# Performance work log

Measured on AMD Instinct MI355X. Metric: run time of the kernel, lower is better.

## Reference

```python
import jax, jax.numpy as jnp
import numpy as np

N_NODES = 50000
N_EDGES = 800000
NUM_REL = 3
NUM_GRAPHS = 512


def _rgcn(x, src, dst, edge_type, Wrel, Wroot, b):
    # PyG RGCNConv with default aggr='mean':
    # out[i] = x[i] @ Wroot + b + sum_r mean_{j in N_r(i)} x[j] @ Wrel[r]
    out = x @ Wroot + b
    for r in range(NUM_REL):
        mask = (edge_type == r)
        h = x @ Wrel[r]                      # transform nodes first (N x d), cheaper than per-edge
        msg = jnp.where(mask[:, None], h[src], jnp.zeros((), x.dtype))  # [E, hid]
        sums = jax.ops.segment_sum(msg, dst, num_segments=N_NODES)
        cnt = jax.ops.segment_sum(mask.astype(x.dtype), dst, num_segments=N_NODES)
        out = out + sums / jnp.maximum(cnt, 1.0)[:, None]
    return out


def setup_inputs() -> dict:
    key = jax.random.key(0)
    ks = jax.random.split(key, 12)
    d, hid, classes = 96, 96, 16
    x = jax.random.normal(ks[0], (N_NODES, d), dtype=jnp.float32)
    edge_index = jax.random.randint(ks[1], (2, N_EDGES), 0, N_NODES, dtype=jnp.int64)
    edge_type = jax.random.randint(ks[2], (N_EDGES,), 0, NUM_REL, dtype=jnp.int64)
    batch = jnp.sort(jax.random.randint(ks[3], (N_NODES,), 0, NUM_GRAPHS, dtype=jnp.int64))
    s1 = 1.0 / np.sqrt(d)
    s2 = 1.0 / np.sqrt(hid)
    return {
        "x": x,
        "edge_index": edge_index,
        "edge_type": edge_type,
        "batch": batch,
        "Wrel1": jax.random.normal(ks[4], (NUM_REL, d, hid), dtype=jnp.float32) * s1,
        "Wroot1": jax.random.normal(ks[5], (d, hid), dtype=jnp.float32) * s1,
        "b1": jnp.zeros((hid,), dtype=jnp.float32),
        "Wrel2": jax.random.normal(ks[6], (NUM_REL, hid, hid), dtype=jnp.float32) * s2,
        "Wroot2": jax.random.normal(ks[7], (hid, hid), dtype=jnp.float32) * s2,
        "b2": jnp.zeros((hid,), dtype=jnp.float32),
        "Wlin": jax.random.normal(ks[8], (hid, classes), dtype=jnp.float32) * s2,
        "blin": jnp.zeros((classes,), dtype=jnp.float32),
    }


def reference(x, edge_index, edge_type, batch, Wrel1, Wroot1, b1, Wrel2, Wroot2, b2, Wlin, blin):
    src, dst = edge_index[0], edge_index[1]
    h = jax.nn.relu(_rgcn(x, src, dst, edge_type, Wrel1, Wroot1, b1))
    h = jax.nn.relu(_rgcn(h, src, dst, edge_type, Wrel2, Wroot2, b2))
    # global mean pool over graphs
    sums = jax.ops.segment_sum(h, batch, num_segments=NUM_GRAPHS)          # [G, hid]
    cnt = jax.ops.segment_sum(jnp.ones((h.shape[0],), h.dtype), batch, num_segments=NUM_GRAPHS)
    pooled = sums / jnp.maximum(cnt, 1.0)[:, None]
    return pooled @ Wlin + blin
```

## Files before the change

### kernel.cpp

```cpp
#include <hip/hip_runtime.h>


#define THREADS 256

typedef __attribute__((ext_vector_type(8))) short short8v;
typedef __attribute__((ext_vector_type(4))) float f32x4;

__device__ __forceinline__ unsigned short f2bf(float f) {
  union { float f; unsigned u; } v; v.f = f;
  unsigned r = v.u + 0x7FFF + ((v.u >> 16) & 1);
  return (unsigned short)(r >> 16);
}
__device__ __forceinline__ float bf2f(unsigned short b) {
  union { unsigned u; float f; } v; v.u = ((unsigned)b) << 16;
  return v.f;
}
__device__ __forceinline__ float bits2f(unsigned u) {
  union { unsigned u; float f; } v; v.u = u;
  return v.f;
}
__device__ __forceinline__ unsigned packbf(float a, float b) {
  return ((unsigned)f2bf(b) << 16) | f2bf(a);
}

__global__ __launch_bounds__(256) void k_prep(
    const float* __restrict__ Wrel1, const float* __restrict__ Wroot1,
    const float* __restrict__ Wrel2, const float* __restrict__ Wroot2,
    unsigned short* __restrict__ PBh, unsigned short* __restrict__ PBl,
    const int* __restrict__ ei, const int* __restrict__ et,
    int* __restrict__ cnt, int* __restrict__ rank, int* __restrict__ bucket,
    int E, int N)
{
  int bid = blockIdx.x;
  if (bid < 288) {
    int lay = bid / 144;
    int idx = (bid % 144) * 256 + threadIdx.x;
    const float* Wroot = lay ? Wroot2 : Wroot1;
    const float* Wrel  = lay ? Wrel2  : Wrel1;
    int j    = idx & 7;
    int lane = (idx >> 3) & 63;
    int CT   = (idx >> 9) % 24;
    int ks   = (idx >> 9) / 24;
    int kpos = ks * 32 + (lane >> 4) * 8 + j;
    int k    = lay ? ((kpos % 6) * 16 + kpos / 6) : kpos;
    int col  = CT * 16 + (lane & 15);
    int m    = col / 96, jj = col % 96;
    float f  = (m == 0) ? Wroot[k * 96 + jj]
                        : Wrel[((size_t)(m - 1) * 96 + k) * 96 + jj];
    unsigned short h = f2bf(f);
    PBh[(size_t)lay * 36864 + idx] = h;
    PBl[(size_t)lay * 36864 + idx] = f2bf(f - bf2f(h));
  } else {
    int e = (bid - 288) * 256 + threadIdx.x;
    if (e >= E) return;
    int b = et[e] * N + ei[E + e];
    bucket[e] = b;
    rank[e] = atomicAdd(&cnt[b], 1);
  }
}

__global__ __launch_bounds__(256) void k_scan1(int* __restrict__ data, int* __restrict__ blockSums)
{
  __shared__ int sh[256];
  int tid = threadIdx.x;
  size_t base = (size_t)blockIdx.x * 1024 + (size_t)tid * 4;
  int4 v = *(const int4*)(data + base);
  int i0 = v.x, i1 = i0 + v.y, i2 = i1 + v.z, i3 = i2 + v.w;
  int tsum = i3;
  sh[tid] = tsum;
  __syncthreads();
  for (int off = 1; off < 256; off <<= 1) {
    int t = (tid >= off) ? sh[tid - off] : 0;
    __syncthreads();
    sh[tid] += t;
    __syncthreads();
  }
  int excl = sh[tid] - tsum;
  int4 o; o.x = i0 + excl; o.y = i1 + excl; o.z = i2 + excl; o.w = i3 + excl;
  *(int4*)(data + base) = o;
  if (tid == 255) blockSums[blockIdx.x] = sh[255];
}

__global__ __launch_bounds__(256) void k_scan2(const int* __restrict__ blockSums,
                                               int* __restrict__ blockOffs, int nb)
{
  __shared__ int sh[256];
  int tid = threadIdx.x;
  int v = (tid < nb) ? blockSums[tid] : 0;
  sh[tid] = v;
  __syncthreads();
  for (int off = 1; off < 256; off <<= 1) {
    int t = (tid >= off) ? sh[tid - off] : 0;
    __syncthreads();
    sh[tid] += t;
    __syncthreads();
  }
  blockOffs[tid] = sh[tid] - v;
}

__global__ __launch_bounds__(256) void k_scan3(int* __restrict__ data, const int* __restrict__ blockOffs)
{
  int tid = threadIdx.x;
  size_t base = (size_t)blockIdx.x * 1024 + (size_t)tid * 4;
  int add = blockOffs[blockIdx.x];
  int4 v = *(const int4*)(data + base);
  v.x += add; v.y += add; v.z += add; v.w += add;
  *(int4*)(data + base) = v;
}

__global__ __launch_bounds__(256) void k_scatter(
    const int* __restrict__ ei, const int* __restrict__ offs,
    const int* __restrict__ rank, const int* __restrict__ bucket,
    unsigned short* __restrict__ payload, int E)
{
  int e = blockIdx.x * THREADS + threadIdx.x;
  if (e >= E) return;
  int b = bucket[e];
  int base = (b == 0) ? 0 : offs[b - 1];
  payload[base + rank[e]] = (unsigned short)ei[e];
}

template<bool F32IN>
__global__ __launch_bounds__(256) void k_gemm(
    const void* __restrict__ Xin_, const unsigned short* __restrict__ Xl,
    const unsigned short* __restrict__ PBh, const unsigned short* __restrict__ PBl,
    float* __restrict__ Yroot, unsigned short* __restrict__ Hrel, int nRows)
{
  int wv = threadIdx.x >> 6, lane = threadIdx.x & 63;
  int lr = lane & 15, lq = lane >> 4;
  int r0 = blockIdx.x * 64;

  f32x4 acc[4][6];
#pragma unroll
  for (int rt = 0; rt < 4; ++rt)
#pragma unroll
    for (int ct = 0; ct < 6; ++ct) acc[rt][ct] = (f32x4){0.f, 0.f, 0.f, 0.f};

#pragma unroll 1
  for (int ks = 0; ks < 3; ++ks) {
    short8v Ah[4], Al[4];
#pragma unroll
    for (int rt = 0; rt < 4; ++rt) {
      int row = r0 + rt * 16 + lr;
      if (row >= nRows) row = nRows - 1;
      size_t off = (size_t)row * 96 + ks * 32 + lq * 8;
      if (F32IN) {
        const float4* xp = (const float4*)((const float*)Xin_ + off);
        float4 va = xp[0], vb = xp[1];
        float vv[8] = {va.x, va.y, va.z, va.w, vb.x, vb.y, vb.z, vb.w};
#pragma unroll
        for (int j = 0; j < 8; ++j) {
          unsigned short h = f2bf(vv[j]);
          Ah[rt][j] = (short)h;
          Al[rt][j] = (short)f2bf(vv[j] - bf2f(h));
        }
      } else {
        Ah[rt] = *(const short8v*)((const unsigned short*)Xin_ + off);
        Al[rt] = *(const short8v*)(Xl + off);
      }
    }
#pragma unroll
    for (int ct = 0; ct < 6; ++ct) {
      int CT = wv * 6 + ct;
      size_t boff = ((size_t)(ks * 24 + CT) * 64 + lane) * 8;
      short8v Bh = *(const short8v*)(PBh + boff);
      short8v Bl = *(const short8v*)(PBl + boff);
#pragma unroll
      for (int rt = 0; rt < 4; ++rt) {
        acc[rt][ct] = __builtin_amdgcn_mfma_f32_16x16x32_bf16(Ah[rt], Bh, acc[rt][ct], 0, 0, 0);
        acc[rt][ct] = __builtin_amdgcn_mfma_f32_16x16x32_bf16(Al[rt], Bh, acc[rt][ct], 0, 0, 0);
        acc[rt][ct] = __builtin_amdgcn_mfma_f32_16x16x32_bf16(Ah[rt], Bl, acc[rt][ct], 0, 0, 0);
      }
    }
  }

  if (wv == 0) {
#pragma unroll
    for (int rt = 0; rt < 4; ++rt)
#pragma unroll
      for (int q = 0; q < 4; ++q) {
        int row = r0 + rt * 16 + lq * 4 + q;
        if (row < nRows) {
          float2* yp = (float2*)(Yroot + (size_t)row * 96 + lr * 6);
          yp[0] = make_float2(acc[rt][0][q], acc[rt][1][q]);
          yp[1] = make_float2(acc[rt][2][q], acc[rt][3][q]);
          yp[2] = make_float2(acc[rt][4][q], acc[rt][5][q]);
        }
      }
  } else {
    int r = wv - 1;
#pragma unroll
    for (int rt = 0; rt < 4; ++rt)
#pragma unroll
      for (int q = 0; q < 4; ++q) {
        int row = r0 + rt * 16 + lq * 4 + q;
        if (row < nRows) {
          unsigned* hp = (unsigned*)(Hrel + ((size_t)r * nRows + row) * 96 + lr * 6);
          hp[0] = packbf(acc[rt][0][q], acc[rt][1][q]);
          hp[1] = packbf(acc[rt][2][q], acc[rt][3][q]);
          hp[2] = packbf(acc[rt][4][q], acc[rt][5][q]);
        }
      }
  }
}

__global__ __launch_bounds__(256) void k_agg3(
    const float* __restrict__ Yroot, const unsigned short* __restrict__ Hrel,
    const int* __restrict__ offs, const unsigned short* __restrict__ payload,
    const float* __restrict__ bias,
    unsigned int* outH, unsigned int* outL, unsigned int* outF, int N)
{
  int node = blockIdx.x * 16 + (threadIdx.x >> 4);
  int l = threadIdx.x & 15;
  if (node >= N) return;

  const float2* yp = (const float2*)(Yroot + (size_t)node * 96) + 3 * l;
  float2 y0 = yp[0], y1 = yp[1], y2 = yp[2];
  float v[6];
  v[0] = y0.x + bias[l];       v[1] = y0.y + bias[16 + l];
  v[2] = y1.x + bias[32 + l];  v[3] = y1.y + bias[48 + l];
  v[4] = y2.x + bias[64 + l];  v[5] = y2.y + bias[80 + l];

#pragma unroll
  for (int r = 0; r < 3; ++r) {
    int bkt = r * N + node;
    int s = (bkt == 0) ? 0 : offs[bkt - 1];
    int e = offs[bkt];
    const unsigned int* base = (const unsigned int*)(Hrel + (size_t)r * N * 96);
    float a[6] = {0.f, 0.f, 0.f, 0.f, 0.f, 0.f};
    int t = s;
    for (; t + 3 < e; t += 4) {
      int p0 = payload[t], p1 = payload[t + 1], p2 = payload[t + 2], p3 = payload[t + 3];
      const unsigned int* h0 = base + (size_t)p0 * 48 + 3 * l;
      const unsigned int* h1 = base + (size_t)p1 * 48 + 3 * l;
      const unsigned int* h2 = base + (size_t)p2 * 48 + 3 * l;
      const unsigned int* h3 = base + (size_t)p3 * 48 + 3 * l;
      unsigned u0 = h0[0], u1 = h0[1], u2 = h0[2];
      unsigned w0 = h1[0], w1 = h1[1], w2 = h1[2];
      unsigned x0 = h2[0], x1 = h2[1], x2 = h2[2];
      unsigned z0 = h3[0], z1 = h3[1], z2 = h3[2];
      a[0] += bits2f(u0 << 16); a[1] += bits2f(u0 & 0xFFFF0000u);
      a[2] += bits2f(u1 << 16); a[3] += bits2f(u1 & 0xFFFF0000u);
      a[4] += bits2f(u2 << 16); a[5] += bits2f(u2 & 0xFFFF0000u);
      a[0] += bits2f(w0 << 16); a[1] += bits2f(w0 & 0xFFFF0000u);
      a[2] += bits2f(w1 << 16); a[3] += bits2f(w1 & 0xFFFF0000u);
      a[4] += bits2f(w2 << 16); a[5] += bits2f(w2 & 0xFFFF0000u);
      a[0] += bits2f(x0 << 16); a[1] += bits2f(x0 & 0xFFFF0000u);
      a[2] += bits2f(x1 << 16); a[3] += bits2f(x1 & 0xFFFF0000u);
      a[4] += bits2f(x2 << 16); a[5] += bits2f(x2 & 0xFFFF0000u);
      a[0] += bits2f(z0 << 16); a[1] += bits2f(z0 & 0xFFFF0000u);
      a[2] += bits2f(z1 << 16); a[3] += bits2f(z1 & 0xFFFF0000u);
      a[4] += bits2f(z2 << 16); a[5] += bits2f(z2 & 0xFFFF0000u);
    }
    for (; t < e; ++t) {
      const unsigned int* h0 = base + (size_t)payload[t] * 48 + 3 * l;
      unsigned u0 = h0[0], u1 = h0[1], u2 = h0[2];
      a[0] += bits2f(u0 << 16); a[1] += bits2f(u0 & 0xFFFF0000u);
      a[2] += bits2f(u1 << 16); a[3] += bits2f(u1 & 0xFFFF0000u);
      a[4] += bits2f(u2 << 16); a[5] += bits2f(u2 & 0xFFFF0000u);
    }
    float inv = (e > s) ? 1.0f / (float)(e - s) : 0.0f;
#pragma unroll
    for (int i = 0; i < 6; ++i) v[i] += a[i] * inv;
  }
#pragma unroll
  for (int i = 0; i < 6; ++i) v[i] = fmaxf(v[i], 0.f);

  size_t ob = (size_t)node * 48 + 3 * l;
  if (outF) {
    outF[ob]     = packbf(v[0], v[1]);
    outF[ob + 1] = packbf(v[2], v[3]);
    outF[ob + 2] = packbf(v[4], v[5]);
  } else {
    unsigned short h[6], lo[6];
#pragma unroll
    for (int i = 0; i < 6; ++i) { h[i] = f2bf(v[i]); lo[i] = f2bf(v[i] - bf2f(h[i])); }
    outH[ob]     = ((unsigned)h[1] << 16) | h[0];
    outH[ob + 1] = ((unsigned)h[3] << 16) | h[2];
    outH[ob + 2] = ((unsigned)h[5] << 16) | h[4];
    outL[ob]     = ((unsigned)lo[1] << 16) | lo[0];
    outL[ob + 1] = ((unsigned)lo[3] << 16) | lo[2];
    outL[ob + 2] = ((unsigned)lo[5] << 16) | lo[4];
  }
}

__global__ __launch_bounds__(256) void k_poolfinal(
    const unsigned int* __restrict__ H, const int* __restrict__ batch,
    const float* __restrict__ Wlin, const float* __restrict__ blin,
    float* __restrict__ out, int N, int G)
{
  int g = blockIdx.x;
  int tid = threadIdx.x;
  int lo = 0, hi = N;
  while (lo < hi) { int m = (lo + hi) >> 1; if (batch[m] < g) lo = m + 1; else hi = m; }
  int s = lo; hi = N;
  while (lo < hi) { int m = (lo + hi) >> 1; if (batch[m] < g + 1) lo = m + 1; else hi = m; }
  int e = lo;

  int grp = tid >> 4, l = tid & 15;
  float a[6] = {0.f, 0.f, 0.f, 0.f, 0.f, 0.f};
  for (int i = s + grp; i < e; i += 16) {
    const unsigned int* hp = H + (size_t)i * 48 + 3 * l;
    unsigned u0 = hp[0], u1 = hp[1], u2 = hp[2];
    a[0] += bits2f(u0 << 16); a[1] += bits2f(u0 & 0xFFFF0000u);
    a[2] += bits2f(u1 << 16); a[3] += bits2f(u1 & 0xFFFF0000u);
    a[4] += bits2f(u2 << 16); a[5] += bits2f(u2 & 0xFFFF0000u);
  }
  __shared__ float sh[16][96];
  __shared__ float pooled[96];
#pragma unroll
  for (int i = 0; i < 6; ++i) sh[grp][6 * l + i] = a[i];
  __syncthreads();
  if (tid < 96) {
    float t = 0.f;
#pragma unroll
    for (int j = 0; j < 16; ++j) t += sh[j][tid];
    float inv = (e > s) ? 1.0f / (float)(e - s) : 0.0f;
    pooled[tid] = t * inv;
  }
  __syncthreads();
  if (tid < 16) {
    float acc = blin[tid];
#pragma unroll
    for (int k = 0; k < 96; ++k)
      acc = fmaf(pooled[k], Wlin[((k % 6) * 16 + k / 6) * 16 + tid], acc);
    out[(size_t)g * 16 + tid] = acc;
  }
}

extern "C" void kernel_launch(void* const* d_in, const int* in_sizes, int n_in,
                              void* d_out, int out_size, void* d_ws, size_t ws_size,
                              hipStream_t stream)
{
  const float* x      = (const float*)d_in[0];
  const int*   ei     = (const int*)d_in[1];
  const int*   et     = (const int*)d_in[2];
  const int*   batch  = (const int*)d_in[3];
  const float* Wrel1  = (const float*)d_in[4];
  const float* Wroot1 = (const float*)d_in[5];
  const float* b1     = (const float*)d_in[6];
  const float* Wrel2  = (const float*)d_in[7];
  const float* Wroot2 = (const float*)d_in[8];
  const float* b2     = (const float*)d_in[9];
  const float* Wlin   = (const float*)d_in[10];
  const float* blin   = (const float*)d_in[11];
  float* out = (float*)d_out;
  (void)n_in; (void)ws_size;

  int N = in_sizes[0] / 96;
  int E = in_sizes[1] / 2;
  int G = out_size / 16;
  int NB = 3 * N;
  int nb1 = (NB + 1023) / 1024;
  int SCAN = nb1 * 1024;

  char* w = (char*)d_ws;
  size_t o = 0;
  auto carve = [&](size_t bytes) -> char* {
    char* p = w + o;
    o = (o + bytes + 255) & ~(size_t)255;
    return p;
  };
  float*          Yroot = (float*)carve((size_t)N * 96 * 4);
  unsigned short* Hrel  = (unsigned short*)carve((size_t)3 * N * 96 * 2);
  unsigned short* Xh    = (unsigned short*)carve((size_t)N * 96 * 2);
  unsigned short* Xl    = (unsigned short*)carve((size_t)N * 96 * 2);
  unsigned short* Hout  = (unsigned short*)carve((size_t)N * 96 * 2);
  unsigned short* PBh   = (unsigned short*)carve((size_t)2 * 36864 * 2);
  unsigned short* PBl   = (unsigned short*)carve((size_t)2 * 36864 * 2);
  int*            offs  = (int*)carve((size_t)SCAN * 4);
  int*            blockSums = (int*)carve(256 * 4);
  int*            blockOffs = (int*)carve(256 * 4);
  int*            rank  = (int*)carve((size_t)E * 4);
  int*            bucket= (int*)carve((size_t)E * 4);
  unsigned short* payload = (unsigned short*)carve((size_t)E * 2);

  hipMemsetAsync(offs, 0, (size_t)SCAN * 4, stream);

  int histBlocks = (E + THREADS - 1) / THREADS;
  k_prep<<<288 + histBlocks, THREADS, 0, stream>>>(
      Wrel1, Wroot1, Wrel2, Wroot2, PBh, PBl, ei, et, offs, rank, bucket, E, N);
  k_scan1<<<nb1, THREADS, 0, stream>>>(offs, blockSums);
  k_scan2<<<1, THREADS, 0, stream>>>(blockSums, blockOffs, nb1);
  k_scan3<<<nb1, THREADS, 0, stream>>>(offs, blockOffs);
  k_scatter<<<histBlocks, THREADS, 0, stream>>>(ei, offs, rank, bucket, payload, E);

  int gg = (N + 63) / 64;
  int ag = (N + 15) / 16;

  k_gemm<true><<<gg, THREADS, 0, stream>>>(x, nullptr, PBh, PBl, Yroot, Hrel, N);
  k_agg3<<<ag, THREADS, 0, stream>>>(Yroot, Hrel, offs, payload, b1,
                                     (unsigned int*)Xh, (unsigned int*)Xl, nullptr, N);
  k_gemm<false><<<gg, THREADS, 0, stream>>>(Xh, Xl, PBh + 36864, PBl + 36864, Yroot, Hrel, N);
  k_agg3<<<ag, THREADS, 0, stream>>>(Yroot, Hrel, offs, payload, b2,
                                     nullptr, nullptr, (unsigned int*)Hout, N);

  k_poolfinal<<<G, THREADS, 0, stream>>>((const unsigned int*)Hout, batch, Wlin, blin, out, N, G);
}
```

Baseline: 292.1 us.

## Stage GEMM A tile in swizzled LDS, interleave hi/lo rows, fuse scan kernels

The GEMM now loads each block's 64-row A tile once into XOR-swizzled shared memory with coalesced 16-byte loads. The fp32 input is split into bf16 hi/lo halves during that staging, and the MFMA loop reads its fragments from LDS instead of doing strided global loads per k-step. The layer-1 aggregation writes hi and lo into one interleaved row buffer so layer-2 GEMM reads a single contiguous 384-byte row. The separate block-offset scan kernel is folded into the add-offset kernel, which costs a redundant 256-element scan in every block but saves one launch. A 24KB LDS tile and launch_bounds(256,4) may limit occupancy.

```diff
diff --git a/kernel.cpp b/kernel.cpp
--- a/kernel.cpp
+++ b/kernel.cpp
@@ -81,8 +81,8 @@
   if (tid == 255) blockSums[blockIdx.x] = sh[255];
 }
 
-__global__ __launch_bounds__(256) void k_scan2(const int* __restrict__ blockSums,
-                                               int* __restrict__ blockOffs, int nb)
+__global__ __launch_bounds__(256) void k_scan3(int* __restrict__ data,
+                                               const int* __restrict__ blockSums, int nb)
 {
   __shared__ int sh[256];
   int tid = threadIdx.x;
@@ -95,17 +95,11 @@
     sh[tid] += t;
     __syncthreads();
   }
-  blockOffs[tid] = sh[tid] - v;
-}
-
-__global__ __launch_bounds__(256) void k_scan3(int* __restrict__ data, const int* __restrict__ blockOffs)
-{
-  int tid = threadIdx.x;
+  int add = (blockIdx.x == 0) ? 0 : sh[blockIdx.x - 1];
   size_t base = (size_t)blockIdx.x * 1024 + (size_t)tid * 4;
-  int add = blockOffs[blockIdx.x];
-  int4 v = *(const int4*)(data + base);
-  v.x += add; v.y += add; v.z += add; v.w += add;
-  *(int4*)(data + base) = v;
+  int4 d = *(const int4*)(data + base);
+  d.x += add; d.y += add; d.z += add; d.w += add;
+  *(int4*)(data + base) = d;
 }
 
 __global__ __launch_bounds__(256) void k_scatter(
@@ -121,44 +115,57 @@
 }
 
 template<bool F32IN>
-__global__ __launch_bounds__(256) void k_gemm(
-    const void* __restrict__ Xin_, const unsigned short* __restrict__ Xl,
+__global__ __launch_bounds__(256, 4) void k_gemm(
+    const void* __restrict__ Xin_,
     const unsigned short* __restrict__ PBh, const unsigned short* __restrict__ PBl,
     float* __restrict__ Yroot, unsigned short* __restrict__ Hrel, int nRows)
 {
-  int wv = threadIdx.x >> 6, lane = threadIdx.x & 63;
+  __shared__ char Als[64 * 384];
+  int tid = threadIdx.x;
+  int wv = tid >> 6, lane = tid & 63;
   int lr = lane & 15, lq = lane >> 4;
   int r0 = blockIdx.x * 64;
 
+  if (F32IN) {
+    const float* Xf = (const float*)Xin_;
+#pragma unroll
+    for (int it = 0; it < 6; ++it) {
+      int chunkId = it * 256 + tid;
+      int row = chunkId / 24, p = chunkId % 24;
+      int grow = r0 + row; if (grow >= nRows) grow = nRows - 1;
+      float4 f = *(const float4*)(Xf + (size_t)grow * 96 + p * 4);
+      unsigned short h0 = f2bf(f.x), h1 = f2bf(f.y), h2 = f2bf(f.z), h3 = f2bf(f.w);
+      unsigned hi0 = ((unsigned)h1 << 16) | h0;
+      unsigned hi1 = ((unsigned)h3 << 16) | h2;
+      unsigned lo0 = ((unsigned)f2bf(f.y - bf2f(h1)) << 16) | f2bf(f.x - bf2f(h0));
+      unsigned lo1 = ((unsigned)f2bf(f.w - bf2f(h3)) << 16) | f2bf(f.z - bf2f(h2));
+      int base = row * 384, xo = row & 7, sub = (p & 1) * 8, ch = p >> 1;
+      *(uint2*)(&Als[base + (((ch     ) ^ xo) << 4) + sub]) = make_uint2(hi0, hi1);
+      *(uint2*)(&Als[base + (((ch + 12) ^ xo) << 4) + sub]) = make_uint2(lo0, lo1);
+    }
+  } else {
+    const char* Xb = (const char*)Xin_;
+#pragma unroll
+    for (int it = 0; it < 6; ++it) {
+      int chunkId = it * 256 + tid;
+      int row = chunkId / 24, c = chunkId % 24;
+      int grow = r0 + row; if (grow >= nRows) grow = nRows - 1;
+      uint4 v = *(const uint4*)(Xb + (size_t)grow * 384 + c * 16);
+      *(uint4*)(&Als[row * 384 + ((c ^ (row & 7)) << 4)]) = v;
+    }
+  }
+  __syncthreads();
+
   f32x4 acc[4][6];
 #pragma unroll
   for (int rt = 0; rt < 4; ++rt)
 #pragma unroll
     for (int ct = 0; ct < 6; ++ct) acc[rt][ct] = (f32x4){0.f, 0.f, 0.f, 0.f};
 
-#pragma unroll 1
+  int xo = lr & 7;
+#pragma unroll
   for (int ks = 0; ks < 3; ++ks) {
-    short8v Ah[4], Al[4];
-#pragma unroll
-    for (int rt = 0; rt < 4; ++rt) {
-      int row = r0 + rt * 16 + lr;
-      if (row >= nRows) row = nRows - 1;
-      size_t off = (size_t)row * 96 + ks * 32 + lq * 8;
-      if (F32IN) {
-        const float4* xp = (const float4*)((const float*)Xin_ + off);
-        float4 va = xp[0], vb = xp[1];
-        float vv[8] = {va.x, va.y, va.z, va.w, vb.x, vb.y, vb.z, vb.w};
-#pragma unroll
-        for (int j = 0; j < 8; ++j) {
-          unsigned short h = f2bf(vv[j]);
-          Ah[rt][j] = (short)h;
-          Al[rt][j] = (short)f2bf(vv[j] - bf2f(h));
-        }
-      } else {
-        Ah[rt] = *(const short8v*)((const unsigned short*)Xin_ + off);
-        Al[rt] = *(const short8v*)(Xl + off);
-      }
-    }
+    int chH = (ks * 4 + lq);
 #pragma unroll
     for (int ct = 0; ct < 6; ++ct) {
       int CT = wv * 6 + ct;
@@ -167,9 +174,12 @@
       short8v Bl = *(const short8v*)(PBl + boff);
 #pragma unroll
       for (int rt = 0; rt < 4; ++rt) {
-        acc[rt][ct] = __builtin_amdgcn_mfma_f32_16x16x32_bf16(Ah[rt], Bh, acc[rt][ct], 0, 0, 0);
-        acc[rt][ct] = __builtin_amdgcn_mfma_f32_16x16x32_bf16(Al[rt], Bh, acc[rt][ct], 0, 0, 0);
-        acc[rt][ct] = __builtin_amdgcn_mfma_f32_16x16x32_bf16(Ah[rt], Bl, acc[rt][ct], 0, 0, 0);
+        int rowb = (rt * 16 + lr) * 384;
+        short8v Ah = *(const short8v*)(&Als[rowb + (((chH     ) ^ xo) << 4)]);
+        short8v Al = *(const short8v*)(&Als[rowb + (((chH + 12) ^ xo) << 4)]);
+        acc[rt][ct] = __builtin_amdgcn_mfma_f32_16x16x32_bf16(Ah, Bh, acc[rt][ct], 0, 0, 0);
+        acc[rt][ct] = __builtin_amdgcn_mfma_f32_16x16x32_bf16(Al, Bh, acc[rt][ct], 0, 0, 0);
+        acc[rt][ct] = __builtin_amdgcn_mfma_f32_16x16x32_bf16(Ah, Bl, acc[rt][ct], 0, 0, 0);
       }
     }
   }
@@ -208,7 +218,7 @@
     const float* __restrict__ Yroot, const unsigned short* __restrict__ Hrel,
     const int* __restrict__ offs, const unsigned short* __restrict__ payload,
     const float* __restrict__ bias,
-    unsigned int* outH, unsigned int* outL, unsigned int* outF, int N)
+    unsigned int* outI, unsigned int* outF, int N)
 {
   int node = blockIdx.x * 16 + (threadIdx.x >> 4);
   int l = threadIdx.x & 15;
@@ -266,8 +276,8 @@
 #pragma unroll
   for (int i = 0; i < 6; ++i) v[i] = fmaxf(v[i], 0.f);
 
-  size_t ob = (size_t)node * 48 + 3 * l;
   if (outF) {
+    size_t ob = (size_t)node * 48 + 3 * l;
     outF[ob]     = packbf(v[0], v[1]);
     outF[ob + 1] = packbf(v[2], v[3]);
     outF[ob + 2] = packbf(v[4], v[5]);
@@ -275,12 +285,13 @@
     unsigned short h[6], lo[6];
 #pragma unroll
     for (int i = 0; i < 6; ++i) { h[i] = f2bf(v[i]); lo[i] = f2bf(v[i] - bf2f(h[i])); }
-    outH[ob]     = ((unsigned)h[1] << 16) | h[0];
-    outH[ob + 1] = ((unsigned)h[3] << 16) | h[2];
-    outH[ob + 2] = ((unsigned)h[5] << 16) | h[4];
-    outL[ob]     = ((unsigned)lo[1] << 16) | lo[0];
-    outL[ob + 1] = ((unsigned)lo[3] << 16) | lo[2];
-    outL[ob + 2] = ((unsigned)lo[5] << 16) | lo[4];
+    unsigned* xp = outI + (size_t)node * 96;
+    xp[3 * l]     = ((unsigned)h[1] << 16) | h[0];
+    xp[3 * l + 1] = ((unsigned)h[3] << 16) | h[2];
+    xp[3 * l + 2] = ((unsigned)h[5] << 16) | h[4];
+    xp[48 + 3 * l]     = ((unsigned)lo[1] << 16) | lo[0];
+    xp[48 + 3 * l + 1] = ((unsigned)lo[3] << 16) | lo[2];
+    xp[48 + 3 * l + 2] = ((unsigned)lo[5] << 16) | lo[4];
   }
 }
 
@@ -363,14 +374,12 @@
   };
   float*          Yroot = (float*)carve((size_t)N * 96 * 4);
   unsigned short* Hrel  = (unsigned short*)carve((size_t)3 * N * 96 * 2);
-  unsigned short* Xh    = (unsigned short*)carve((size_t)N * 96 * 2);
-  unsigned short* Xl    = (unsigned short*)carve((size_t)N * 96 * 2);
-  unsigned short* Hout  = (unsigned short*)carve((size_t)N * 96 * 2);
+  unsigned int*   X2    = (unsigned int*)carve((size_t)N * 96 * 4);
+  unsigned int*   Hout  = (unsigned int*)carve((size_t)N * 48 * 4);
   unsigned short* PBh   = (unsigned short*)carve((size_t)2 * 36864 * 2);
   unsigned short* PBl   = (unsigned short*)carve((size_t)2 * 36864 * 2);
   int*            offs  = (int*)carve((size_t)SCAN * 4);
   int*            blockSums = (int*)carve(256 * 4);
-  int*            blockOffs = (int*)carve(256 * 4);
   int*            rank  = (int*)carve((size_t)E * 4);
   int*            bucket= (int*)carve((size_t)E * 4);
   unsigned short* payload = (unsigned short*)carve((size_t)E * 2);
@@ -381,19 +390,18 @@
   k_prep<<<288 + histBlocks, THREADS, 0, stream>>>(
       Wrel1, Wroot1, Wrel2, Wroot2, PBh, PBl, ei, et, offs, rank, bucket, E, N);
   k_scan1<<<nb1, THREADS, 0, stream>>>(offs, blockSums);
-  k_scan2<<<1, THREADS, 0, stream>>>(blockSums, blockOffs, nb1);
-  k_scan3<<<nb1, THREADS, 0, stream>>>(offs, blockOffs);
+  k_scan3<<<nb1, THREADS, 0, stream>>>(offs, blockSums, nb1);
   k_scatter<<<histBlocks, THREADS, 0, stream>>>(ei, offs, rank, bucket, payload, E);
 
   int gg = (N + 63) / 64;
   int ag = (N + 15) / 16;
 
-  k_gemm<true><<<gg, THREADS, 0, stream>>>(x, nullptr, PBh, PBl, Yroot, Hrel, N);
+  k_gemm<true><<<gg, THREADS, 0, stream>>>(x, PBh, PBl, Yroot, Hrel, N);
   k_agg3<<<ag, THREADS, 0, stream>>>(Yroot, Hrel, offs, payload, b1,
-                                     (unsigned int*)Xh, (unsigned int*)Xl, nullptr, N);
-  k_gemm<false><<<gg, THREADS, 0, stream>>>(Xh, Xl, PBh + 36864, PBl + 36864, Yroot, Hrel, N);
+                                     X2, nullptr, N);
+  k_gemm<false><<<gg, THREADS, 0, stream>>>(X2, PBh + 36864, PBl + 36864, Yroot, Hrel, N);
   k_agg3<<<ag, THREADS, 0, stream>>>(Yroot, Hrel, offs, payload, b2,
-                                     nullptr, nullptr, (unsigned int*)Hout, N);
-
-  k_poolfinal<<<G, THREADS, 0, stream>>>((const unsigned int*)Hout, batch, Wlin, blin, out, N, G);
-}
+                                     nullptr, Hout, N);
+
+  k_poolfinal<<<G, THREADS, 0, stream>>>(Hout, batch, Wlin, blin, out, N, G);
+}
```

After: 295.4 us. About the same (+1.1%).
